# Kernel optimization log

Hardware: AMD Instinct MI355X
Metric: run time of the kernel (lower is better)

## Reference

```python
import jax, jax.numpy as jnp
import numpy as np

N_ENT, N_REL, D, H, N_MID = 4096, 200, 128, 4, 9  # 1 input layer + 9 middle layers + 1 out layer
ALPHA = 0.2
NEG = -9e15


def gat_head(x, adj_mask, W, a):
    # x: [N, Fin], W: [Fin, Fout], a: [2*Fout]
    Wh = x @ W                                   # [N, Fout]
    d = Wh.shape[-1]
    f1 = Wh @ a[:d]                              # [N]
    f2 = Wh @ a[d:]                              # [N]
    e = jax.nn.leaky_relu(f1[:, None] + f2[None, :], ALPHA)  # [N, N]
    e = jnp.where(adj_mask, e, NEG)
    attn = jax.nn.softmax(e, axis=-1)
    return attn @ Wh                             # [N, Fout]


def multihead_concat(x, adj_mask, Ws, As):
    # Ws: [H, Fin, Fout], As: [H, 2*Fout] -> elu(concat over heads) [N, H*Fout]
    heads = jax.vmap(lambda W, a: gat_head(x, adj_mask, W, a))(Ws, As)  # [H, N, Fout]
    N = x.shape[0]
    return jax.nn.elu(jnp.transpose(heads, (1, 0, 2)).reshape(N, -1))


def setup_inputs() -> dict:
    key = jax.random.key(0)
    ks = jax.random.split(key, 12)
    s = 0.1
    return {
        "head": jax.random.randint(ks[0], (4096,), 0, N_ENT),
        "relation": jax.random.randint(ks[1], (4096,), 0, N_REL),
        "adj": jax.random.normal(ks[2], (N_ENT, N_ENT), dtype=jnp.float32),
        "entity_emb": jax.random.normal(ks[3], (N_ENT, D), dtype=jnp.float32) * s,
        "relation_emb": jax.random.normal(ks[4], (N_REL, D), dtype=jnp.float32) * s,
        "W0": jax.random.normal(ks[5], (H, D, D), dtype=jnp.float32) * s,
        "a0": jax.random.normal(ks[6], (H, 2 * D), dtype=jnp.float32) * s,
        "Wm": jax.random.normal(ks[7], (N_MID, H, H * D, D), dtype=jnp.float32) * s,
        "am": jax.random.normal(ks[8], (N_MID, H, 2 * D), dtype=jnp.float32) * s,
        "Wo": jax.random.normal(ks[9], (H * D, D), dtype=jnp.float32) * s,
        "ao": jax.random.normal(ks[10], (2 * D,), dtype=jnp.float32) * s,
    }


def reference(head, relation, adj, entity_emb, relation_emb, W0, a0, Wm, am, Wo, ao):
    adj_mask = adj > 0
    # layer 0: D -> H*D
    x = multihead_concat(entity_emb, adj_mask, W0, a0)
    # 9 middle layers: H*D -> H*D (identical shapes -> scan)
    def step(x, params):
        Ws, As = params
        return multihead_concat(x, adj_mask, Ws, As), None
    x, _ = jax.lax.scan(step, x, (Wm, am))
    # output layer: single head H*D -> D, elu applied after
    x = jax.nn.elu(gat_head(x, adj_mask, Wo, ao))
    head_relation_combined = entity_emb[head] + relation_emb[relation]
    return (x, head_relation_combined)
```

## Files before the change

### kernel.cpp

```cpp
#include <hip/hip_runtime.h>

typedef unsigned short u16;
typedef short bf16x8 __attribute__((ext_vector_type(8)));
typedef float f32x4 __attribute__((ext_vector_type(4)));

__device__ __forceinline__ float bf2f(unsigned v) { return __uint_as_float(v << 16); }
__device__ __forceinline__ u16 f2bf(float f) {
    unsigned u = __float_as_uint(f);
    return (u16)((u + 0x7fffu + ((u >> 16) & 1u)) >> 16);
}

__device__ __forceinline__ void gload_lds16(const void* g, void* l) {
    __builtin_amdgcn_global_load_lds(
        (const __attribute__((address_space(1))) unsigned int*)g,
        (__attribute__((address_space(3))) unsigned int*)l, 16, 0, 0);
}

__global__ __launch_bounds__(256) void k_mask(const float* __restrict__ adj,
                                              unsigned* __restrict__ mask) {
    int w = blockIdx.x * 256 + threadIdx.x;
    const float4* q = (const float4*)(adj + (size_t)w * 32);
    unsigned bits = 0u;
#pragma unroll
    for (int i = 0; i < 8; i++) {
        float4 v = q[i];
        if (v.x > 0.f) bits |= (1u << (i * 4 + 0));
        if (v.y > 0.f) bits |= (1u << (i * 4 + 1));
        if (v.z > 0.f) bits |= (1u << (i * 4 + 2));
        if (v.w > 0.f) bits |= (1u << (i * 4 + 3));
    }
    mask[w] = bits;
}

__global__ void k_trans(const float* __restrict__ in, u16* __restrict__ out, int K) {
    __shared__ float t[32][33];
    const float* src = in + (size_t)blockIdx.z * K * 128;
    u16* dst = out + (size_t)blockIdx.z * K * 128;
    int k0 = blockIdx.x * 32, n0 = blockIdx.y * 32;
    int tx = threadIdx.x, ty = threadIdx.y;
#pragma unroll
    for (int i = 0; i < 32; i += 8) t[ty + i][tx] = src[(size_t)(k0 + ty + i) * 128 + n0 + tx];
    __syncthreads();
#pragma unroll
    for (int i = 0; i < 32; i += 8) dst[(size_t)(n0 + ty + i) * K + k0 + tx] = f2bf(t[tx][ty + i]);
}

__global__ __launch_bounds__(256) void k_cvt(const float* __restrict__ in,
                                             u16* __restrict__ out) {
    int t = blockIdx.x * 256 + threadIdx.x;
    float4 v = ((const float4*)in)[t];
    uint2 o;
    o.x = (unsigned)f2bf(v.x) | ((unsigned)f2bf(v.y) << 16);
    o.y = (unsigned)f2bf(v.z) | ((unsigned)f2bf(v.w) << 16);
    ((uint2*)out)[t] = o;
}

__global__ __launch_bounds__(1024, 4) void k_proj(const u16* __restrict__ X,
                                                  const u16* __restrict__ WT,
                                                  const float* __restrict__ avec,
                                                  u16* __restrict__ WhT,
                                                  float* __restrict__ f1,
                                                  float* __restrict__ f2, int Fin) {
    __shared__ u16 As[2][64 * 32];
    __shared__ u16 Bs[2][128 * 32];
    __shared__ float fpart[4][64][2];
    const int tid = threadIdx.x;
    const int wv = tid >> 6, lane = tid & 63;
    const int rg = wv & 3, cg = wv >> 2;
    const int c = lane & 15, quad = lane >> 4;
    const int h = blockIdx.y;
    const int j0 = blockIdx.x * 64;
    const u16* Wp = WT + (size_t)h * 128 * Fin;

#define PROJ_STAGE(buf, kb)                                                              \
    do {                                                                                 \
        if (cg == 0)                                                                     \
            gload_lds16(X + (size_t)(j0 + rg * 16 + (lane >> 2)) * Fin + (kb) + (lane & 3) * 8, \
                        (void*)&As[buf][rg * 16 * 32]);                                  \
        else if (cg <= 2)                                                                \
            gload_lds16(Wp + (size_t)((cg - 1) * 64 + rg * 16 + (lane >> 2)) * Fin + (kb) + (lane & 3) * 8, \
                        (void*)&Bs[buf][((cg - 1) * 64 + rg * 16) * 32]);                \
    } while (0)

    PROJ_STAGE(0, 0);
    __syncthreads();

    f32x4 acc[2];
    acc[0] = (f32x4){0.f, 0.f, 0.f, 0.f};
    acc[1] = (f32x4){0.f, 0.f, 0.f, 0.f};

    int it = 0;
    for (int kb = 0; kb < Fin; kb += 32, it++) {
        const int cur = it & 1;
        if (kb + 32 < Fin) PROJ_STAGE(cur ^ 1, kb + 32);
        bf16x8 av = *(const bf16x8*)&As[cur][(rg * 16 + c) * 32 + quad * 8];
#pragma unroll
        for (int e = 0; e < 2; e++) {
            bf16x8 bv = *(const bf16x8*)&Bs[cur][((cg * 2 + e) * 16 + c) * 32 + quad * 8];
            acc[e] = __builtin_amdgcn_mfma_f32_16x16x32_bf16(av, bv, acc[e], 0, 0, 0);
        }
        __syncthreads();
    }

    u16* Wo = WhT + (size_t)h * 128 * 4096;
    const float* ah = avec + h * 256;
    float p1[4] = {0, 0, 0, 0}, p2[4] = {0, 0, 0, 0};
#pragma unroll
    for (int e = 0; e < 2; e++) {
        const int n = (cg * 2 + e) * 16 + c;
        float a1 = ah[n];
        float a2 = ah[128 + n];
        u16 w4[4];
#pragma unroll
        for (int r = 0; r < 4; r++) {
            float v = acc[e][r];
            w4[r] = f2bf(v);
            p1[r] += v * a1;
            p2[r] += v * a2;
        }
        uint2 pk;
        pk.x = (unsigned)w4[0] | ((unsigned)w4[1] << 16);
        pk.y = (unsigned)w4[2] | ((unsigned)w4[3] << 16);
        *(uint2*)&Wo[(size_t)n * 4096 + j0 + rg * 16 + quad * 4] = pk;
    }
#pragma unroll
    for (int off = 1; off < 16; off <<= 1) {
#pragma unroll
        for (int r = 0; r < 4; r++) {
            p1[r] += __shfl_xor(p1[r], off);
            p2[r] += __shfl_xor(p2[r], off);
        }
    }
    if (c == 0) {
#pragma unroll
        for (int r = 0; r < 4; r++) {
            fpart[cg][rg * 16 + quad * 4 + r][0] = p1[r];
            fpart[cg][rg * 16 + quad * 4 + r][1] = p2[r];
        }
    }
    __syncthreads();
    if (tid < 64) {
        float s1 = fpart[0][tid][0] + fpart[1][tid][0] + fpart[2][tid][0] + fpart[3][tid][0];
        float s2 = fpart[0][tid][1] + fpart[1][tid][1] + fpart[2][tid][1] + fpart[3][tid][1];
        f1[h * 4096 + j0 + tid] = s1;
        f2[h * 4096 + j0 + tid] = s2;
    }
}

template <bool F32OUT>
__global__ __launch_bounds__(1024, 4) void k_attn(const u16* __restrict__ WhT,
                                                  const float* __restrict__ f1g,
                                                  const float* __restrict__ f2g,
                                                  const unsigned char* __restrict__ maskb,
                                                  void* __restrict__ outp, int ostride) {
    __shared__ float f2s[4096];
    __shared__ unsigned char ms[64 * 528];
    __shared__ u16 Bs[2][4][128 * 32];
    __shared__ float f1s[64];
    __shared__ float lpart[4][64];
    __shared__ float redmax[16];
    __shared__ float red[64 * 132];

    const int tid = threadIdx.x;
    const int wv = tid >> 6, lane = tid & 63;
    const int jg = wv >> 2, rg = wv & 3;
    const int c = lane & 15, quad = lane >> 4;
    const int h = blockIdx.y;
    const int i0 = blockIdx.x * 64;
    const float LOG2E = 1.4426950408889634f;
    const float* f1h = f1g + h * 4096;
    const float* f2h = f2g + h * 4096;
    const u16* Wp = WhT + (size_t)h * 128 * 4096;

#define ATTN_STAGE(buf, kb)                                                              \
    do {                                                                                 \
        const int jb_ = jg * 1024 + (kb) * 32;                                           \
        _Pragma("unroll")                                                                \
        for (int e = 0; e < 2; e++)                                                      \
            gload_lds16(Wp + (size_t)(rg * 32 + e * 16 + (lane >> 2)) * 4096 + jb_ + (lane & 3) * 8, \
                        (void*)&Bs[buf][jg][(rg * 32 + e * 16) * 32]);                   \
    } while (0)

    float mymax = -3.0e38f;
    {
        float4 v = ((const float4*)f2h)[tid];
        v.x *= LOG2E; v.y *= LOG2E; v.z *= LOG2E; v.w *= LOG2E;
        ((float4*)f2s)[tid] = v;
        mymax = fmaxf(fmaxf(v.x, v.y), fmaxf(v.z, v.w));
    }
    if (tid < 64) f1s[tid] = f1h[i0 + tid] * LOG2E;
    {
        const uint4* msrc = (const uint4*)(maskb + (size_t)i0 * 512);
#pragma unroll
        for (int e = 0; e < 2; e++) {
            int o = tid + e * 1024;
            uint4 v = msrc[o];
            int row = o >> 5, col = o & 31;
            *(uint4*)&ms[row * 528 + col * 16] = v;
        }
    }
    ATTN_STAGE(0, 0);
#pragma unroll
    for (int off = 1; off < 64; off <<= 1) mymax = fmaxf(mymax, __shfl_xor(mymax, off));
    if (lane == 0) redmax[wv] = mymax;
    __syncthreads();
    float F2MAX = redmax[0];
#pragma unroll
    for (int i = 1; i < 16; i++) F2MAX = fmaxf(F2MAX, redmax[i]);

    const int iloc = rg * 16 + c;
    const float rf1 = f1s[iloc];
    const float zb = rf1 + F2MAX;
    const float rm = fmaxf(zb, 0.2f * zb);
    const float Ac = rf1 - rm;
    const float Bc = 0.2f * rf1 - rm;

    f32x4 acc[8];
#pragma unroll
    for (int i = 0; i < 8; i++) acc[i] = (f32x4){0.f, 0.f, 0.f, 0.f};
    float lsum = 0.f;

    for (int kb = 0; kb < 32; kb++) {
        const int cur = kb & 1;
        if (kb < 31) ATTN_STAGE(cur ^ 1, kb + 1);
        const int jb = jg * 1024 + kb * 32;
        const unsigned mb = ms[iloc * 528 + jg * 128 + kb * 4 + quad];
        const float4 fa = *(const float4*)&f2s[jb + quad * 8];
        const float4 fb = *(const float4*)&f2s[jb + quad * 8 + 4];
        const float f2v[8] = {fa.x, fa.y, fa.z, fa.w, fb.x, fb.y, fb.z, fb.w};
        union { bf16x8 v; unsigned u[4]; } af;
#pragma unroll
        for (int t = 0; t < 8; t += 2) {
            float s0 = fmaxf(Ac + f2v[t],     __builtin_fmaf(0.2f, f2v[t],     Bc));
            float s1 = fmaxf(Ac + f2v[t + 1], __builtin_fmaf(0.2f, f2v[t + 1], Bc));
            float p0 = __builtin_amdgcn_exp2f(s0);
            float p1 = __builtin_amdgcn_exp2f(s1);
            unsigned u0 = ((mb >> t) & 1u)       ? (__float_as_uint(p0) & 0xffff0000u) : 0u;
            unsigned u1 = ((mb >> (t + 1)) & 1u) ? (__float_as_uint(p1) & 0xffff0000u) : 0u;
            lsum += __uint_as_float(u0) + __uint_as_float(u1);
            af.u[t >> 1] = (u0 >> 16) | u1;
        }
#pragma unroll
        for (int nt = 0; nt < 8; nt++) {
            bf16x8 bv = *(const bf16x8*)&Bs[cur][jg][(nt * 16 + c) * 32 + quad * 8];
            acc[nt] = __builtin_amdgcn_mfma_f32_16x16x32_bf16(af.v, bv, acc[nt], 0, 0, 0);
        }
        __syncthreads();
    }

    lsum += __shfl_xor(lsum, 16);
    lsum += __shfl_xor(lsum, 32);
    if (quad == 0) lpart[jg][iloc] = lsum;

#pragma unroll
    for (int g = 0; g < 4; g++) {
        __syncthreads();
        if (jg == g) {
#pragma unroll
            for (int nt = 0; nt < 8; nt++) {
#pragma unroll
                for (int r = 0; r < 4; r++) {
                    int idx = (rg * 16 + quad * 4 + r) * 132 + nt * 16 + c;
                    if (g == 0) red[idx] = acc[nt][r];
                    else        red[idx] += acc[nt][r];
                }
            }
        }
    }
    __syncthreads();

    const int row = tid >> 4, cb = tid & 15;
    const float l = lpart[0][row] + lpart[1][row] + lpart[2][row] + lpart[3][row];
    const float linv = 1.0f / l;
    float vv[8];
#pragma unroll
    for (int t = 0; t < 8; t++) {
        float v = red[row * 132 + cb * 8 + t] * linv;
        vv[t] = v > 0.f ? v : __expf(v) - 1.f;
    }
    const size_t obase = (size_t)(i0 + row) * ostride + h * 128 + cb * 8;
    if (F32OUT) {
        float* op = (float*)outp + obase;
        *(float4*)op = *(float4*)&vv[0];
        *(float4*)(op + 4) = *(float4*)&vv[4];
    } else {
        uint4 o;
        o.x = (unsigned)f2bf(vv[0]) | ((unsigned)f2bf(vv[1]) << 16);
        o.y = (unsigned)f2bf(vv[2]) | ((unsigned)f2bf(vv[3]) << 16);
        o.z = (unsigned)f2bf(vv[4]) | ((unsigned)f2bf(vv[5]) << 16);
        o.w = (unsigned)f2bf(vv[6]) | ((unsigned)f2bf(vv[7]) << 16);
        *(uint4*)((u16*)outp + obase) = o;
    }
}

__global__ __launch_bounds__(256) void k_gather(const int* __restrict__ head,
                                                const int* __restrict__ rel,
                                                const float* __restrict__ ent,
                                                const float* __restrict__ rele,
                                                float* __restrict__ out) {
    int t = blockIdx.x * 256 + threadIdx.x;
    int row = t >> 5, sg = t & 31;
    int hh = head[row], rr = rel[row];
    float4 a = ((const float4*)(ent + (size_t)hh * 128))[sg];
    float4 b = ((const float4*)(rele + (size_t)rr * 128))[sg];
    float4 o;
    o.x = a.x + b.x; o.y = a.y + b.y; o.z = a.z + b.z; o.w = a.w + b.w;
    ((float4*)(out + (size_t)row * 128))[sg] = o;
}

extern "C" void kernel_launch(void* const* d_in, const int* in_sizes, int n_in,
                              void* d_out, int out_size, void* d_ws, size_t ws_size,
                              hipStream_t stream) {
    const int*   head = (const int*)d_in[0];
    const int*   rel  = (const int*)d_in[1];
    const float* adj  = (const float*)d_in[2];
    const float* ent  = (const float*)d_in[3];
    const float* rele = (const float*)d_in[4];
    const float* W0   = (const float*)d_in[5];
    const float* a0   = (const float*)d_in[6];
    const float* Wm   = (const float*)d_in[7];
    const float* am   = (const float*)d_in[8];
    const float* Wo   = (const float*)d_in[9];
    const float* ao   = (const float*)d_in[10];

    char* ws = (char*)d_ws;
    unsigned* mask = (unsigned*)(ws + 0);
    u16* WT0 = (u16*)(ws + 2097152);
    u16* WT5 = (u16*)(ws + 2228224);
    u16* WhT = (u16*)(ws + 7077888);
    float* f1 = (float*)(ws + 11272192);
    float* f2 = (float*)(ws + 11337728);
    u16* xA = (u16*)(ws + 11403264);
    u16* xB = (u16*)(ws + 15597568);
    u16* x0 = (u16*)(ws + 19791872);

    float* out_x = (float*)d_out;
    float* out_comb = out_x + (size_t)4096 * 128;

    k_mask<<<2048, 256, 0, stream>>>(adj, mask);
    k_cvt<<<512, 256, 0, stream>>>(ent, x0);
    k_trans<<<dim3(4, 4, 4), dim3(32, 8), 0, stream>>>(W0, WT0, 128);
    k_trans<<<dim3(16, 4, 36), dim3(32, 8), 0, stream>>>(Wm, WT5, 512);
    k_trans<<<dim3(16, 4, 1), dim3(32, 8), 0, stream>>>(Wo, WT5 + (size_t)36 * 512 * 128, 512);
    k_gather<<<512, 256, 0, stream>>>(head, rel, ent, rele, out_comb);

    k_proj<<<dim3(64, 4), 1024, 0, stream>>>(x0, WT0, a0, WhT, f1, f2, 128);
    k_attn<false><<<dim3(64, 4), 1024, 0, stream>>>(WhT, f1, f2, (const unsigned char*)mask, xA, 512);
    u16 *xc = xA, *xn = xB;
    for (int l = 0; l < 9; l++) {
        k_proj<<<dim3(64, 4), 1024, 0, stream>>>(xc, WT5 + (size_t)l * 4 * 512 * 128,
                                                 am + (size_t)l * 4 * 256, WhT, f1, f2, 512);
        k_attn<false><<<dim3(64, 4), 1024, 0, stream>>>(WhT, f1, f2, (const unsigned char*)mask, xn, 512);
        u16* t = xc; xc = xn; xn = t;
    }
    k_proj<<<dim3(64, 1), 1024, 0, stream>>>(xc, WT5 + (size_t)36 * 512 * 128, ao, WhT, f1, f2, 512);
    k_attn<true><<<dim3(64, 1), 1024, 0, stream>>>(WhT, f1, f2, (const unsigned char*)mask, out_x, 128);
}
```

Measured before the change: 670.8 us.

## Factor attention exponentials into per-column precomputed exp pairs and swizzle LDS

The projection kernel now emits exp2(f2) and exp2(0.2*f2) per column, and the attention kernel rebuilds each masked softmax weight as a per-row constant times one of these, chosen by comparing against exp2(-f1). This removes the per-element exp and the global f2 max reduction. Row sums are computed with an extra MFMA against a ones vector instead of scalar adds. LDS tiles get an XOR swizzle to cut bank conflicts, the loop is unrolled by two with register prefetch of the exp pairs, and the reduction buffer reuses the Bs area to save LDS. Dropping the max subtraction risks overflow or underflow in the factored exponentials.

```diff
diff --git a/kernel.cpp b/kernel.cpp
--- a/kernel.cpp
+++ b/kernel.cpp
@@ -15,6 +15,7 @@
         (const __attribute__((address_space(1))) unsigned int*)g,
         (__attribute__((address_space(3))) unsigned int*)l, 16, 0, 0);
 }
+
 
 __global__ __launch_bounds__(256) void k_mask(const float* __restrict__ adj,
                                               unsigned* __restrict__ mask) {
@@ -60,7 +61,7 @@
                                                   const float* __restrict__ avec,
                                                   u16* __restrict__ WhT,
                                                   float* __restrict__ f1,
-                                                  float* __restrict__ f2, int Fin) {
+                                                  float* __restrict__ E12g, int Fin) {
     __shared__ u16 As[2][64 * 32];
     __shared__ u16 Bs[2][128 * 32];
     __shared__ float fpart[4][64][2];
@@ -68,17 +69,19 @@
     const int wv = tid >> 6, lane = tid & 63;
     const int rg = wv & 3, cg = wv >> 2;
     const int c = lane & 15, quad = lane >> 4;
+    const int bofs = (quad ^ ((c >> 1) & 3)) * 8;
     const int h = blockIdx.y;
     const int j0 = blockIdx.x * 64;
     const u16* Wp = WT + (size_t)h * 128 * Fin;
+    const int sgr = ((lane & 3) ^ ((lane >> 3) & 3)) * 8;
 
 #define PROJ_STAGE(buf, kb)                                                              \
     do {                                                                                 \
         if (cg == 0)                                                                     \
-            gload_lds16(X + (size_t)(j0 + rg * 16 + (lane >> 2)) * Fin + (kb) + (lane & 3) * 8, \
+            gload_lds16(X + (size_t)(j0 + rg * 16 + (lane >> 2)) * Fin + (kb) + sgr,     \
                         (void*)&As[buf][rg * 16 * 32]);                                  \
         else if (cg <= 2)                                                                \
-            gload_lds16(Wp + (size_t)((cg - 1) * 64 + rg * 16 + (lane >> 2)) * Fin + (kb) + (lane & 3) * 8, \
+            gload_lds16(Wp + (size_t)((cg - 1) * 64 + rg * 16 + (lane >> 2)) * Fin + (kb) + sgr, \
                         (void*)&Bs[buf][((cg - 1) * 64 + rg * 16) * 32]);                \
     } while (0)
 
@@ -93,10 +96,10 @@
     for (int kb = 0; kb < Fin; kb += 32, it++) {
         const int cur = it & 1;
         if (kb + 32 < Fin) PROJ_STAGE(cur ^ 1, kb + 32);
-        bf16x8 av = *(const bf16x8*)&As[cur][(rg * 16 + c) * 32 + quad * 8];
+        bf16x8 av = *(const bf16x8*)&As[cur][(rg * 16 + c) * 32 + bofs];
 #pragma unroll
         for (int e = 0; e < 2; e++) {
-            bf16x8 bv = *(const bf16x8*)&Bs[cur][((cg * 2 + e) * 16 + c) * 32 + quad * 8];
+            bf16x8 bv = *(const bf16x8*)&Bs[cur][((cg * 2 + e) * 16 + c) * 32 + bofs];
             acc[e] = __builtin_amdgcn_mfma_f32_16x16x32_bf16(av, bv, acc[e], 0, 0, 0);
         }
         __syncthreads();
@@ -143,52 +146,44 @@
         float s1 = fpart[0][tid][0] + fpart[1][tid][0] + fpart[2][tid][0] + fpart[3][tid][0];
         float s2 = fpart[0][tid][1] + fpart[1][tid][1] + fpart[2][tid][1] + fpart[3][tid][1];
         f1[h * 4096 + j0 + tid] = s1;
-        f2[h * 4096 + j0 + tid] = s2;
+        const float LOG2E = 1.4426950408889634f;
+        float d = s2 * LOG2E;
+        float* e12 = E12g + h * 8192 + 2 * (j0 + tid);
+        e12[0] = __builtin_amdgcn_exp2f(d);
+        e12[1] = __builtin_amdgcn_exp2f(0.2f * d);
     }
 }
 
 template <bool F32OUT>
 __global__ __launch_bounds__(1024, 4) void k_attn(const u16* __restrict__ WhT,
                                                   const float* __restrict__ f1g,
-                                                  const float* __restrict__ f2g,
+                                                  const float* __restrict__ E12g,
                                                   const unsigned char* __restrict__ maskb,
                                                   void* __restrict__ outp, int ostride) {
-    __shared__ float f2s[4096];
     __shared__ unsigned char ms[64 * 528];
     __shared__ u16 Bs[2][4][128 * 32];
-    __shared__ float f1s[64];
     __shared__ float lpart[4][64];
-    __shared__ float redmax[16];
-    __shared__ float red[64 * 132];
 
     const int tid = threadIdx.x;
     const int wv = tid >> 6, lane = tid & 63;
     const int jg = wv >> 2, rg = wv & 3;
     const int c = lane & 15, quad = lane >> 4;
+    const int bofs = (quad ^ ((c >> 1) & 3)) * 8;
+    const int sgr = ((lane & 3) ^ ((lane >> 3) & 3)) * 8;
     const int h = blockIdx.y;
     const int i0 = blockIdx.x * 64;
     const float LOG2E = 1.4426950408889634f;
-    const float* f1h = f1g + h * 4096;
-    const float* f2h = f2g + h * 4096;
     const u16* Wp = WhT + (size_t)h * 128 * 4096;
 
 #define ATTN_STAGE(buf, kb)                                                              \
     do {                                                                                 \
         const int jb_ = jg * 1024 + (kb) * 32;                                           \
         _Pragma("unroll")                                                                \
-        for (int e = 0; e < 2; e++)                                                      \
-            gload_lds16(Wp + (size_t)(rg * 32 + e * 16 + (lane >> 2)) * 4096 + jb_ + (lane & 3) * 8, \
-                        (void*)&Bs[buf][jg][(rg * 32 + e * 16) * 32]);                   \
+        for (int e_ = 0; e_ < 2; e_++)                                                   \
+            gload_lds16(Wp + (size_t)(rg * 32 + e_ * 16 + (lane >> 2)) * 4096 + jb_ + sgr, \
+                        (void*)&Bs[buf][jg][(rg * 32 + e_ * 16) * 32]);                  \
     } while (0)
 
-    float mymax = -3.0e38f;
-    {
-        float4 v = ((const float4*)f2h)[tid];
-        v.x *= LOG2E; v.y *= LOG2E; v.z *= LOG2E; v.w *= LOG2E;
-        ((float4*)f2s)[tid] = v;
-        mymax = fmaxf(fmaxf(v.x, v.y), fmaxf(v.z, v.w));
-    }
-    if (tid < 64) f1s[tid] = f1h[i0 + tid] * LOG2E;
     {
         const uint4* msrc = (const uint4*)(maskb + (size_t)i0 * 512);
 #pragma unroll
@@ -200,58 +195,91 @@
         }
     }
     ATTN_STAGE(0, 0);
-#pragma unroll
-    for (int off = 1; off < 64; off <<= 1) mymax = fmaxf(mymax, __shfl_xor(mymax, off));
-    if (lane == 0) redmax[wv] = mymax;
-    __syncthreads();
-    float F2MAX = redmax[0];
-#pragma unroll
-    for (int i = 1; i < 16; i++) F2MAX = fmaxf(F2MAX, redmax[i]);
 
     const int iloc = rg * 16 + c;
-    const float rf1 = f1s[iloc];
-    const float zb = rf1 + F2MAX;
-    const float rm = fmaxf(zb, 0.2f * zb);
-    const float Ac = rf1 - rm;
-    const float Bc = 0.2f * rf1 - rm;
+    const float rf1 = f1g[h * 4096 + i0 + iloc] * LOG2E;
+    const float rm = fmaxf(rf1, 0.2f * rf1);
+    const float C1 = __builtin_amdgcn_exp2f(rf1 - rm);
+    const float C2 = __builtin_amdgcn_exp2f(0.2f * rf1 - rm);
+    const float T  = __builtin_amdgcn_exp2f(-rf1);
+
+    const float* ep = E12g + h * 8192 + jg * 2048 + quad * 16;
+    float4 eA[4], eB[4];
+#pragma unroll
+    for (int q = 0; q < 4; q++) eA[q] = *(const float4*)(ep + 0 * 64 + q * 4);
+#pragma unroll
+    for (int q = 0; q < 4; q++) eB[q] = *(const float4*)(ep + 1 * 64 + q * 4);
+
+    bf16x8 onesv;
+#pragma unroll
+    for (int i = 0; i < 8; i++) onesv[i] = (short)0x3F80;
 
     f32x4 acc[8];
 #pragma unroll
     for (int i = 0; i < 8; i++) acc[i] = (f32x4){0.f, 0.f, 0.f, 0.f};
-    float lsum = 0.f;
-
-    for (int kb = 0; kb < 32; kb++) {
-        const int cur = kb & 1;
-        if (kb < 31) ATTN_STAGE(cur ^ 1, kb + 1);
-        const int jb = jg * 1024 + kb * 32;
-        const unsigned mb = ms[iloc * 528 + jg * 128 + kb * 4 + quad];
-        const float4 fa = *(const float4*)&f2s[jb + quad * 8];
-        const float4 fb = *(const float4*)&f2s[jb + quad * 8 + 4];
-        const float f2v[8] = {fa.x, fa.y, fa.z, fa.w, fb.x, fb.y, fb.z, fb.w};
-        union { bf16x8 v; unsigned u[4]; } af;
-#pragma unroll
-        for (int t = 0; t < 8; t += 2) {
-            float s0 = fmaxf(Ac + f2v[t],     __builtin_fmaf(0.2f, f2v[t],     Bc));
-            float s1 = fmaxf(Ac + f2v[t + 1], __builtin_fmaf(0.2f, f2v[t + 1], Bc));
-            float p0 = __builtin_amdgcn_exp2f(s0);
-            float p1 = __builtin_amdgcn_exp2f(s1);
-            unsigned u0 = ((mb >> t) & 1u)       ? (__float_as_uint(p0) & 0xffff0000u) : 0u;
-            unsigned u1 = ((mb >> (t + 1)) & 1u) ? (__float_as_uint(p1) & 0xffff0000u) : 0u;
-            lsum += __uint_as_float(u0) + __uint_as_float(u1);
-            af.u[t >> 1] = (u0 >> 16) | u1;
-        }
-#pragma unroll
-        for (int nt = 0; nt < 8; nt++) {
-            bf16x8 bv = *(const bf16x8*)&Bs[cur][jg][(nt * 16 + c) * 32 + quad * 8];
-            acc[nt] = __builtin_amdgcn_mfma_f32_16x16x32_bf16(af.v, bv, acc[nt], 0, 0, 0);
-        }
+    f32x4 acc_l = (f32x4){0.f, 0.f, 0.f, 0.f};
+
+    union AF { bf16x8 v; unsigned u[4]; };
+    AF afA, afB;
+
+#define COMP_P(dst, mb_, E_)                                                             \
+    do {                                                                                 \
+        _Pragma("unroll")                                                                \
+        for (int t = 0; t < 8; t += 2) {                                                 \
+            float4 e_ = E_[t >> 1];                                                      \
+            float p0 = ((e_.x > T) ? C1 : C2) * ((e_.x > T) ? e_.x : e_.y);              \
+            float p1 = ((e_.z > T) ? C1 : C2) * ((e_.z > T) ? e_.z : e_.w);              \
+            unsigned u0 = ((mb_ >> t) & 1u)       ? (__float_as_uint(p0) & 0xffff0000u) : 0u; \
+            unsigned u1 = ((mb_ >> (t + 1)) & 1u) ? (__float_as_uint(p1) & 0xffff0000u) : 0u; \
+            dst.u[t >> 1] = (u0 >> 16) | u1;                                             \
+        }                                                                                \
+    } while (0)
+
+#define DO_MFMA(src, buf)                                                                \
+    do {                                                                                 \
+        _Pragma("unroll")                                                                \
+        for (int nt = 0; nt < 8; nt++) {                                                 \
+            bf16x8 bv_ = *(const bf16x8*)&Bs[buf][jg][(nt * 16 + c) * 32 + bofs];        \
+            acc[nt] = __builtin_amdgcn_mfma_f32_16x16x32_bf16(src.v, bv_, acc[nt], 0, 0, 0); \
+        }                                                                                \
+        acc_l = __builtin_amdgcn_mfma_f32_16x16x32_bf16(src.v, onesv, acc_l, 0, 0, 0);   \
+    } while (0)
+
+    const unsigned char* mrow = &ms[iloc * 528 + jg * 128 + quad];
+    __syncthreads();
+
+    for (int kb = 0; kb < 32; kb += 2) {
+        ATTN_STAGE(1, kb + 1);
+        {
+            const unsigned mbA = mrow[kb * 4];
+            COMP_P(afA, mbA, eA);
+        }
+        if (kb + 2 < 32) {
+#pragma unroll
+            for (int q = 0; q < 4; q++) eA[q] = *(const float4*)(ep + (kb + 2) * 64 + q * 4);
+        }
+        DO_MFMA(afA, 0);
         __syncthreads();
-    }
-
-    lsum += __shfl_xor(lsum, 16);
-    lsum += __shfl_xor(lsum, 32);
-    if (quad == 0) lpart[jg][iloc] = lsum;
-
+        if (kb + 2 < 32) ATTN_STAGE(0, kb + 2);
+        {
+            const unsigned mbB = mrow[(kb + 1) * 4];
+            COMP_P(afB, mbB, eB);
+        }
+        if (kb + 3 < 32) {
+#pragma unroll
+            for (int q = 0; q < 4; q++) eB[q] = *(const float4*)(ep + (kb + 3) * 64 + q * 4);
+        }
+        DO_MFMA(afB, 1);
+        __syncthreads();
+    }
+
+    if (c == 0) {
+#pragma unroll
+        for (int r = 0; r < 4; r++)
+            lpart[jg][rg * 16 + quad * 4 + r] = acc_l[r];
+    }
+
+    float* red = (float*)&Bs[0][0][0];
 #pragma unroll
     for (int g = 0; g < 4; g++) {
         __syncthreads();
@@ -329,10 +357,10 @@
     u16* WT5 = (u16*)(ws + 2228224);
     u16* WhT = (u16*)(ws + 7077888);
     float* f1 = (float*)(ws + 11272192);
-    float* f2 = (float*)(ws + 11337728);
     u16* xA = (u16*)(ws + 11403264);
     u16* xB = (u16*)(ws + 15597568);
     u16* x0 = (u16*)(ws + 19791872);
+    float* E12 = (float*)(ws + 20840448);
 
     float* out_x = (float*)d_out;
     float* out_comb = out_x + (size_t)4096 * 128;
@@ -344,15 +372,15 @@
     k_trans<<<dim3(16, 4, 1), dim3(32, 8), 0, stream>>>(Wo, WT5 + (size_t)36 * 512 * 128, 512);
     k_gather<<<512, 256, 0, stream>>>(head, rel, ent, rele, out_comb);
 
-    k_proj<<<dim3(64, 4), 1024, 0, stream>>>(x0, WT0, a0, WhT, f1, f2, 128);
-    k_attn<false><<<dim3(64, 4), 1024, 0, stream>>>(WhT, f1, f2, (const unsigned char*)mask, xA, 512);
+    k_proj<<<dim3(64, 4), 1024, 0, stream>>>(x0, WT0, a0, WhT, f1, E12, 128);
+    k_attn<false><<<dim3(64, 4), 1024, 0, stream>>>(WhT, f1, E12, (const unsigned char*)mask, xA, 512);
     u16 *xc = xA, *xn = xB;
     for (int l = 0; l < 9; l++) {
         k_proj<<<dim3(64, 4), 1024, 0, stream>>>(xc, WT5 + (size_t)l * 4 * 512 * 128,
-                                                 am + (size_t)l * 4 * 256, WhT, f1, f2, 512);
-        k_attn<false><<<dim3(64, 4), 1024, 0, stream>>>(WhT, f1, f2, (const unsigned char*)mask, xn, 512);
+                                                 am + (size_t)l * 4 * 256, WhT, f1, E12, 512);
+        k_attn<false><<<dim3(64, 4), 1024, 0, stream>>>(WhT, f1, E12, (const unsigned char*)mask, xn, 512);
         u16* t = xc; xc = xn; xn = t;
     }
-    k_proj<<<dim3(64, 1), 1024, 0, stream>>>(xc, WT5 + (size_t)36 * 512 * 128, ao, WhT, f1, f2, 512);
-    k_attn<true><<<dim3(64, 1), 1024, 0, stream>>>(WhT, f1, f2, (const unsigned char*)mask, out_x, 128);
-}
+    k_proj<<<dim3(64, 1), 1024, 0, stream>>>(xc, WT5 + (size_t)36 * 512 * 128, ao, WhT, f1, E12, 512);
+    k_attn<true><<<dim3(64, 1), 1024, 0, stream>>>(WhT, f1, E12, (const unsigned char*)mask, out_x, 128);
+}
```

Result: slower. 748.4 us (+11.6%).
